# Kernel tuning notes

Measured on AMD Instinct MI355X. Metric: run time of the kernel, lower is better.

Reference implementation:

```python
import jax, jax.numpy as jnp
import numpy as np

NUM_GRAPHS = 512


def setup_inputs() -> dict:
    key = jax.random.key(0)
    ks = jax.random.split(key, 12)
    N, E, D, H, C = 100000, 1600000, 128, 128, 10
    x = jax.random.normal(ks[0], (N, D), dtype=jnp.float32)
    edge_index = jax.random.randint(ks[1], (2, E), 0, N, dtype=jnp.int64)
    batch = jnp.sort(jax.random.randint(ks[2], (N,), 0, NUM_GRAPHS, dtype=jnp.int64))
    def glorot(k, fan_in, fan_out):
        s = jnp.sqrt(6.0 / (fan_in + fan_out))
        return jax.random.uniform(k, (fan_in, fan_out), jnp.float32, -s, s)
    return {
        "x": x, "edge_index": edge_index, "batch": batch,
        "W_init": glorot(ks[3], D, H), "b_init": jnp.zeros((H,), jnp.float32),
        "W_h0": glorot(ks[4], H, H), "b_h0": jnp.zeros((H,), jnp.float32),
        "W_h1": glorot(ks[5], H, H), "b_h1": jnp.zeros((H,), jnp.float32),
        "W_out": glorot(ks[6], H, C), "b_out": jnp.zeros((C,), jnp.float32),
    }


def reference(x, edge_index, batch, W_init, b_init, W_h0, b_h0, W_h1, b_h1, W_out, b_out):
    N = x.shape[0]
    loop = jnp.arange(N, dtype=edge_index.dtype)
    # add self-loops (PyG GCNConv default)
    row = jnp.concatenate([edge_index[0], loop])  # source
    col = jnp.concatenate([edge_index[1], loop])  # target
    # symmetric normalization D^-1/2 (A+I) D^-1/2, degrees on target index
    deg = jax.ops.segment_sum(jnp.ones_like(col, dtype=x.dtype), col, num_segments=N)
    dis = jnp.where(deg > 0, jax.lax.rsqrt(jnp.maximum(deg, 1e-12)), 0.0)
    norm = dis[row] * dis[col]  # [E+N]

    def gcn_conv(h, W, b):
        h = h @ W                                    # linear first (as in PyG)
        msg = h[row] * norm[:, None]                 # gather + scale
        return jax.ops.segment_sum(msg, col, num_segments=N) + b  # scatter-add

    h = jax.nn.relu(gcn_conv(x, W_init, b_init))
    h = jax.nn.relu(gcn_conv(h, W_h0, b_h0))
    h = jax.nn.relu(gcn_conv(h, W_h1, b_h1))
    h = gcn_conv(h, W_out, b_out)
    # global mean pooling over graphs
    sums = jax.ops.segment_sum(h, batch, num_segments=NUM_GRAPHS)
    cnt = jax.ops.segment_sum(jnp.ones((N, 1), h.dtype), batch, num_segments=NUM_GRAPHS)
    return sums / jnp.maximum(cnt, 1.0)
```

## Files before the change

### kernel.cpp

```cpp
#include <hip/hip_runtime.h>


#define SCAN_BLOCKS 64
#define SCAN_THREADS (SCAN_BLOCKS * 256)

typedef unsigned short u16;
typedef unsigned int   u32;
typedef __attribute__((ext_vector_type(8))) short bf16x8;
typedef __attribute__((ext_vector_type(4))) float f32x4;

static __device__ __forceinline__ u16 f2bf(float x) {
    u32 u = __float_as_uint(x);
    u32 r = (u + 0x7fffu + ((u >> 16) & 1u)) >> 16;
    return (u16)r;
}
static __device__ __forceinline__ float bf_lo(u32 p) { return __uint_as_float(p << 16); }
static __device__ __forceinline__ float bf_hi(u32 p) { return __uint_as_float(p & 0xffff0000u); }

__global__ __launch_bounds__(256) void k_count(const int* __restrict__ col, int E,
                                               int* __restrict__ cnt,
                                               u16* __restrict__ rank) {
    int e = blockIdx.x * 256 + threadIdx.x;
    if (e < E) rank[e] = (u16)atomicAdd(&cnt[col[e]], 1);
}

__global__ __launch_bounds__(256) void k_scan1(const int* __restrict__ cnt,
                                               int* __restrict__ tsum, int N) {
    int t = blockIdx.x * 256 + threadIdx.x;
    int strip = (N + SCAN_THREADS - 1) / SCAN_THREADS;
    int s0 = t * strip;
    int s1 = s0 + strip; if (s1 > N) s1 = N;
    int s = 0;
    for (int i = s0; i < s1; ++i) s += (cnt[i] + 3) & ~3;
    tsum[t] = s;
}

__global__ __launch_bounds__(1024) void k_scan2(int* __restrict__ tsum) {
    __shared__ int part[1024];
    int t = threadIdx.x;
    int base = t * 16;
    int local[16];
    int s = 0;
    #pragma unroll
    for (int i = 0; i < 16; ++i) { local[i] = tsum[base + i]; s += local[i]; }
    part[t] = s;
    __syncthreads();
    for (int off = 1; off < 1024; off <<= 1) {
        int v = part[t];
        int add = (t >= off) ? part[t - off] : 0;
        __syncthreads();
        part[t] = v + add;
        __syncthreads();
    }
    int run = (t == 0) ? 0 : part[t - 1];
    #pragma unroll
    for (int i = 0; i < 16; ++i) { int c = local[i]; tsum[base + i] = run; run += c; }
}

__global__ __launch_bounds__(256) void k_scan3(const int* __restrict__ cnt,
                                               const int* __restrict__ tsum,
                                               int* __restrict__ rowptr,
                                               float* __restrict__ dis,
                                               int* __restrict__ csr, int N) {
    int t = blockIdx.x * 256 + threadIdx.x;
    int strip = (N + SCAN_THREADS - 1) / SCAN_THREADS;
    int s0 = t * strip;
    int s1 = s0 + strip; if (s1 > N) s1 = N;
    int run = tsum[t];
    for (int i = s0; i < s1; ++i) {
        int c = cnt[i];
        int r = (c + 3) & ~3;
        rowptr[i] = run;
        for (int p = run + c; p < run + r; ++p) csr[p] = N;
        run += r;
        dis[i] = rsqrtf((float)(c + 1));
    }
    if (t == SCAN_THREADS - 1) rowptr[N] = run;
}

__global__ __launch_bounds__(256) void k_fill(const int* __restrict__ row,
                                              const int* __restrict__ col, int E,
                                              const int* __restrict__ rowptr,
                                              const u16* __restrict__ rank,
                                              int* __restrict__ csr) {
    int e = blockIdx.x * 256 + threadIdx.x;
    if (e < E) {
        int c = col[e];
        csr[rowptr[c] + (int)rank[e]] = row[e];
    }
}

__global__ __launch_bounds__(256) void k_cast(const float* __restrict__ src,
                                              const float* __restrict__ dis,
                                              u16* __restrict__ bX,
                                              u16* __restrict__ bA,
                                              u16* __restrict__ bB, int N) {
    int i = blockIdx.x * 256 + threadIdx.x;
    int total = (N + 1) * 32;
    if (i >= total) return;
    int v = i >> 5;
    if (v < N) {
        float dv = dis[v];
        float4 val = ((const float4*)src)[i];
        ushort4 o;
        o.x = f2bf(dv * val.x); o.y = f2bf(dv * val.y);
        o.z = f2bf(dv * val.z); o.w = f2bf(dv * val.w);
        ((ushort4*)bX)[i] = o;
    } else {
        ushort4 z = {0, 0, 0, 0};
        ((ushort4*)bX)[i] = z;
        ((ushort4*)bA)[i] = z;
        ((ushort4*)bB)[i] = z;
    }
}

__global__ __launch_bounds__(256) void k_wprep4(const float* __restrict__ W0,
                                                const float* __restrict__ W1,
                                                const float* __restrict__ W2,
                                                const float* __restrict__ Wo,
                                                u32* __restrict__ whi,
                                                u32* __restrict__ wlo, int C) {
    if (blockIdx.x < 24) {
        int which = blockIdx.x >> 3;
        const float* W = (which == 0) ? W0 : (which == 1) ? W1 : W2;
        int t = (blockIdx.x & 7) * 256 + threadIdx.x;
        int lane = t & 63;
        int nk = t >> 6;
        int k0 = nk & 3;
        int ntile = nk >> 2;
        int n = ntile * 16 + (lane & 15);
        int kbase = k0 * 32 + (lane >> 4) * 8;
        u32 hi[4], lo[4];
        #pragma unroll
        for (int tt = 0; tt < 4; ++tt) {
            float w0 = W[(kbase + 2 * tt) * 128 + n];
            float w1 = W[(kbase + 2 * tt + 1) * 128 + n];
            u16 h0 = f2bf(w0), h1 = f2bf(w1);
            u16 l0 = f2bf(w0 - __uint_as_float((u32)h0 << 16));
            u16 l1 = f2bf(w1 - __uint_as_float((u32)h1 << 16));
            hi[tt] = (u32)h0 | ((u32)h1 << 16);
            lo[tt] = (u32)l0 | ((u32)l1 << 16);
        }
        uint4 qh = {hi[0], hi[1], hi[2], hi[3]};
        uint4 ql = {lo[0], lo[1], lo[2], lo[3]};
        int base = which * 2048;
        ((uint4*)whi)[base + t] = qh;
        ((uint4*)wlo)[base + t] = ql;
    } else {
        int t = threadIdx.x;
        int lane = t & 63;
        int k0 = t >> 6;
        int n = lane & 15;
        int kbase = k0 * 32 + (lane >> 4) * 8;
        bool vc = (n < C);
        u32 hi[4], lo[4];
        #pragma unroll
        for (int tt = 0; tt < 4; ++tt) {
            float w0 = vc ? Wo[(kbase + 2 * tt) * C + n] : 0.f;
            float w1 = vc ? Wo[(kbase + 2 * tt + 1) * C + n] : 0.f;
            u16 h0 = f2bf(w0), h1 = f2bf(w1);
            u16 l0 = f2bf(w0 - __uint_as_float((u32)h0 << 16));
            u16 l1 = f2bf(w1 - __uint_as_float((u32)h1 << 16));
            hi[tt] = (u32)h0 | ((u32)h1 << 16);
            lo[tt] = (u32)l0 | ((u32)l1 << 16);
        }
        uint4 qh = {hi[0], hi[1], hi[2], hi[3]};
        uint4 ql = {lo[0], lo[1], lo[2], lo[3]};
        ((uint4*)whi)[6144 + t] = qh;
        ((uint4*)wlo)[6144 + t] = ql;
    }
}

__global__ __launch_bounds__(256) void k_fused(const u16* __restrict__ hin,
                                               const u32* __restrict__ whi,
                                               const u32* __restrict__ wlo,
                                               const float* __restrict__ bias,
                                               u16* __restrict__ hout,
                                               const int* __restrict__ rowptr,
                                               const int* __restrict__ csr,
                                               const float* __restrict__ dis,
                                               int N, int scale_out,
                                               int proj,
                                               const u32* __restrict__ pwhi,
                                               const u32* __restrict__ pwlo,
                                               float* __restrict__ tmpC) {
    __shared__ u32 sS[32 * 68];
    __shared__ float dS[32];
    int tid = threadIdx.x;
    int wave = tid >> 6;
    int lane = tid & 63;
    int row0 = blockIdx.x * 32;
    const uint4* hin4 = (const uint4*)hin;

    int grp = lane >> 4;
    int sub = lane & 15;
    #pragma unroll
    for (int jj = 0; jj < 2; ++jj) {
        int rloc = wave * 8 + jj * 4 + grp;
        int row = row0 + rloc;
        bool hR = row < N;
        int ia = 0, rem = 0;
        float dv = 1.f;
        if (hR) {
            ia  = rowptr[row];
            rem = rowptr[row + 1] - ia;
            dv  = dis[row];
        }
        int nself = hR ? row : N;
        uint4 ps = hin4[((u32)nself << 4) + sub];
        float a0 = bf_lo(ps.x), a1 = bf_hi(ps.x);
        float a2 = bf_lo(ps.y), a3 = bf_hi(ps.y);
        float a4 = bf_lo(ps.z), a5 = bf_hi(ps.z);
        float a6 = bf_lo(ps.w), a7 = bf_hi(ps.w);
        int m = rem;
        m = max(m, __shfl_xor(m, 16));
        m = max(m, __shfl_xor(m, 32));
        const int4* cq = (const int4*)(csr + ia);
        for (int k = 0; k < m; k += 8) {
            int4 q0 = cq[(k >> 2)];
            int4 q1 = cq[(k >> 2) + 1];
            bool v0 = k < rem;
            bool v1 = (k + 4) < rem;
            int n0 = v0 ? q0.x : N;
            int n1 = v0 ? q0.y : N;
            int n2 = v0 ? q0.z : N;
            int n3 = v0 ? q0.w : N;
            int n4 = v1 ? q1.x : N;
            int n5 = v1 ? q1.y : N;
            int n6 = v1 ? q1.z : N;
            int n7 = v1 ? q1.w : N;
            uint4 p0 = hin4[((u32)n0 << 4) + sub];
            uint4 p1 = hin4[((u32)n1 << 4) + sub];
            uint4 p2 = hin4[((u32)n2 << 4) + sub];
            uint4 p3 = hin4[((u32)n3 << 4) + sub];
            uint4 p4 = hin4[((u32)n4 << 4) + sub];
            uint4 p5 = hin4[((u32)n5 << 4) + sub];
            uint4 p6 = hin4[((u32)n6 << 4) + sub];
            uint4 p7 = hin4[((u32)n7 << 4) + sub];
            a0 += bf_lo(p0.x) + bf_lo(p1.x) + bf_lo(p2.x) + bf_lo(p3.x);
            a1 += bf_hi(p0.x) + bf_hi(p1.x) + bf_hi(p2.x) + bf_hi(p3.x);
            a2 += bf_lo(p0.y) + bf_lo(p1.y) + bf_lo(p2.y) + bf_lo(p3.y);
            a3 += bf_hi(p0.y) + bf_hi(p1.y) + bf_hi(p2.y) + bf_hi(p3.y);
            a4 += bf_lo(p0.z) + bf_lo(p1.z) + bf_lo(p2.z) + bf_lo(p3.z);
            a5 += bf_hi(p0.z) + bf_hi(p1.z) + bf_hi(p2.z) + bf_hi(p3.z);
            a6 += bf_lo(p0.w) + bf_lo(p1.w) + bf_lo(p2.w) + bf_lo(p3.w);
            a7 += bf_hi(p0.w) + bf_hi(p1.w) + bf_hi(p2.w) + bf_hi(p3.w);
            a0 += bf_lo(p4.x) + bf_lo(p5.x) + bf_lo(p6.x) + bf_lo(p7.x);
            a1 += bf_hi(p4.x) + bf_hi(p5.x) + bf_hi(p6.x) + bf_hi(p7.x);
            a2 += bf_lo(p4.y) + bf_lo(p5.y) + bf_lo(p6.y) + bf_lo(p7.y);
            a3 += bf_hi(p4.y) + bf_hi(p5.y) + bf_hi(p6.y) + bf_hi(p7.y);
            a4 += bf_lo(p4.z) + bf_lo(p5.z) + bf_lo(p6.z) + bf_lo(p7.z);
            a5 += bf_hi(p4.z) + bf_hi(p5.z) + bf_hi(p6.z) + bf_hi(p7.z);
            a6 += bf_lo(p4.w) + bf_lo(p5.w) + bf_lo(p6.w) + bf_lo(p7.w);
            a7 += bf_hi(p4.w) + bf_hi(p5.w) + bf_hi(p6.w) + bf_hi(p7.w);
        }
        u32 w0 = (u32)f2bf(dv * a0) | ((u32)f2bf(dv * a1) << 16);
        u32 w1 = (u32)f2bf(dv * a2) | ((u32)f2bf(dv * a3) << 16);
        u32 w2 = (u32)f2bf(dv * a4) | ((u32)f2bf(dv * a5) << 16);
        u32 w3 = (u32)f2bf(dv * a6) | ((u32)f2bf(dv * a7) << 16);
        sS[rloc * 65 + sub * 4 + 0] = w0;
        sS[rloc * 65 + sub * 4 + 1] = w1;
        sS[rloc * 65 + sub * 4 + 2] = w2;
        sS[rloc * 65 + sub * 4 + 3] = w3;
        if (sub == 0) dS[rloc] = dv;
    }
    __syncthreads();

    f32x4 acc[2][2] = {{{0.f,0.f,0.f,0.f},{0.f,0.f,0.f,0.f}},
                       {{0.f,0.f,0.f,0.f},{0.f,0.f,0.f,0.f}}};
    int mA = lane & 15;
    int qA = lane >> 4;
    #pragma unroll
    for (int k0 = 0; k0 < 4; ++k0) {
        union { u32 u[4]; bf16x8 v; } A0, A1;
        int ub = k0 * 16 + qA * 4;
        #pragma unroll
        for (int tt = 0; tt < 4; ++tt) {
            A0.u[tt] = sS[mA * 65 + ub + tt];
            A1.u[tt] = sS[(mA + 16) * 65 + ub + tt];
        }
        #pragma unroll
        for (int ct = 0; ct < 2; ++ct) {
            int ntk = ((2 * wave + ct) * 4 + k0) * 64 + lane;
            union { uint4 q; bf16x8 v; } BH, BL;
            BH.q = ((const uint4*)whi)[ntk];
            BL.q = ((const uint4*)wlo)[ntk];
            acc[0][ct] = __builtin_amdgcn_mfma_f32_16x16x32_bf16(A0.v, BH.v, acc[0][ct], 0, 0, 0);
            acc[0][ct] = __builtin_amdgcn_mfma_f32_16x16x32_bf16(A0.v, BL.v, acc[0][ct], 0, 0, 0);
            acc[1][ct] = __builtin_amdgcn_mfma_f32_16x16x32_bf16(A1.v, BH.v, acc[1][ct], 0, 0, 0);
            acc[1][ct] = __builtin_amdgcn_mfma_f32_16x16x32_bf16(A1.v, BL.v, acc[1][ct], 0, 0, 0);
        }
    }

    if (!proj) {
        #pragma unroll
        for (int rt = 0; rt < 2; ++rt) {
            #pragma unroll
            for (int ct = 0; ct < 2; ++ct) {
                int col = (2 * wave + ct) * 16 + (lane & 15);
                float bb = bias[col];
                #pragma unroll
                for (int r = 0; r < 4; ++r) {
                    int rloc = rt * 16 + (lane >> 4) * 4 + r;
                    int row = row0 + rloc;
                    if (row < N) {
                        float o = fmaxf(acc[rt][ct][r] + bb, 0.f);
                        if (scale_out) o *= dS[rloc];
                        hout[((u32)row << 7) + col] = f2bf(o);
                    }
                }
            }
        }
    } else {
        __syncthreads();
        u16* hS16 = (u16*)sS;
        #pragma unroll
        for (int rt = 0; rt < 2; ++rt) {
            #pragma unroll
            for (int ct = 0; ct < 2; ++ct) {
                int col = (2 * wave + ct) * 16 + (lane & 15);
                float bb = bias[col];
                #pragma unroll
                for (int r = 0; r < 4; ++r) {
                    int rloc = rt * 16 + (lane >> 4) * 4 + r;
                    hS16[rloc * 136 + col] = f2bf(fmaxf(acc[rt][ct][r] + bb, 0.f));
                }
            }
        }
        __syncthreads();
        if (wave < 2) {
            int m2 = lane & 15;
            int quad = lane >> 4;
            f32x4 a2 = {0.f, 0.f, 0.f, 0.f};
            #pragma unroll
            for (int k0 = 0; k0 < 4; ++k0) {
                bf16x8 Afrag = *(bf16x8*)&hS16[(wave * 16 + m2) * 136 + k0 * 32 + quad * 8];
                union { uint4 q; bf16x8 v; } BH, BL;
                BH.q = ((const uint4*)pwhi)[k0 * 64 + lane];
                BL.q = ((const uint4*)pwlo)[k0 * 64 + lane];
                a2 = __builtin_amdgcn_mfma_f32_16x16x32_bf16(Afrag, BH.v, a2, 0, 0, 0);
                a2 = __builtin_amdgcn_mfma_f32_16x16x32_bf16(Afrag, BL.v, a2, 0, 0, 0);
            }
            #pragma unroll
            for (int r = 0; r < 4; ++r) {
                int rloc = wave * 16 + quad * 4 + r;
                int row = row0 + rloc;
                if (row < N) tmpC[((u32)row << 4) + m2] = a2[r] * dS[rloc];
            }
        }
        if (blockIdx.x == 0 && tid < 16) tmpC[((u32)N << 4) + tid] = 0.f;
    }
}

__global__ __launch_bounds__(256) void k_aggpool(const float* __restrict__ tp,
                                                 const int* __restrict__ rowptr,
                                                 const int* __restrict__ csr,
                                                 const float* __restrict__ dis,
                                                 const int* __restrict__ batch,
                                                 const float* __restrict__ bout,
                                                 float* __restrict__ out,
                                                 int N, int C) {
    __shared__ float red[256];
    int g = blockIdx.x;
    int tid = threadIdx.x;
    int c = tid & 15;
    int rg = tid >> 4;
    int lo = 0, hi = N;
    while (lo < hi) { int m = (lo + hi) >> 1; if (batch[m] < g) lo = m + 1; else hi = m; }
    int lb = lo;
    hi = N;
    while (lo < hi) { int m = (lo + hi) >> 1; if (batch[m] <= g) lo = m + 1; else hi = m; }
    int ub = lo;
    const int4* csr4 = (const int4*)csr;
    float pacc = 0.f;
    for (int v = lb + rg; v < ub; v += 16) {
        float acc = tp[((u32)v << 4) + c];
        int i = rowptr[v], e = rowptr[v + 1];
        for (; i + 8 <= e; i += 8) {
            int4 q0 = csr4[(u32)i >> 2];
            int4 q1 = csr4[((u32)i >> 2) + 1];
            acc += tp[((u32)q0.x << 4) + c] + tp[((u32)q0.y << 4) + c]
                 + tp[((u32)q0.z << 4) + c] + tp[((u32)q0.w << 4) + c]
                 + tp[((u32)q1.x << 4) + c] + tp[((u32)q1.y << 4) + c]
                 + tp[((u32)q1.z << 4) + c] + tp[((u32)q1.w << 4) + c];
        }
        if (i < e) {
            int4 q0 = csr4[(u32)i >> 2];
            acc += tp[((u32)q0.x << 4) + c] + tp[((u32)q0.y << 4) + c]
                 + tp[((u32)q0.z << 4) + c] + tp[((u32)q0.w << 4) + c];
        }
        pacc += dis[v] * acc;
    }
    red[tid] = pacc;
    __syncthreads();
    #pragma unroll
    for (int s = 8; s >= 1; s >>= 1) {
        if (rg < s) red[tid] += red[tid + s * 16];
        __syncthreads();
    }
    if (tid < C) {
        float cnt = (float)(ub - lb);
        out[g * C + tid] = (red[tid] + cnt * bout[tid]) / fmaxf(cnt, 1.0f);
    }
}

extern "C" void kernel_launch(void* const* d_in, const int* in_sizes, int n_in,
                              void* d_out, int out_size, void* d_ws, size_t ws_size,
                              hipStream_t stream) {
    const float* x      = (const float*)d_in[0];
    const int*   ei     = (const int*)d_in[1];
    const int*   batch  = (const int*)d_in[2];
    const float* W_init = (const float*)d_in[3];
    const float* b_init = (const float*)d_in[4];
    const float* W_h0   = (const float*)d_in[5];
    const float* b_h0   = (const float*)d_in[6];
    const float* W_h1   = (const float*)d_in[7];
    const float* b_h1   = (const float*)d_in[8];
    const float* W_out  = (const float*)d_in[9];
    const float* b_out  = (const float*)d_in[10];

    int N = in_sizes[0] / 128;
    int E = in_sizes[1] / 2;
    int C = in_sizes[10];
    int G = out_size / C;

    size_t off = 0;
    auto alloc = [&](size_t bytes) -> char* {
        char* p = (char*)d_ws + off;
        off += (bytes + 255) & ~(size_t)255;
        return p;
    };
    u16*   bufX   = (u16*)  alloc((size_t)(N + 1) * 128 * 2);
    u16*   bufA   = (u16*)  alloc((size_t)(N + 1) * 128 * 2);
    u16*   bufB   = (u16*)  alloc((size_t)(N + 1) * 128 * 2);
    float* dis    = (float*)alloc((size_t)N * 4);
    int*   rowptr = (int*)  alloc((size_t)(N + 1) * 4);
    int*   csr    = (int*)  alloc(((size_t)E + 3 * (size_t)N + 8) * 4);
    int*   tsum   = (int*)  alloc((size_t)SCAN_THREADS * 4);
    u32*   whi    = (u32*)  alloc((3 * 2048 + 256) * 16);
    u32*   wlo    = (u32*)  alloc((3 * 2048 + 256) * 16);
    size_t zoff   = off;
    int*   cnt    = (int*)  alloc((size_t)N * 4);
    size_t zbytes = off - zoff;

    u16*   rank   = (u16*)bufB;
    float* tmpC   = (float*)bufX;

    hipMemsetAsync(cnt, 0, zbytes, stream);

    const int* rowi = ei;
    const int* coli = ei + E;

    int eb = (E + 255) / 256;
    k_count<<<eb, 256, 0, stream>>>(coli, E, cnt, rank);
    k_scan1<<<SCAN_BLOCKS, 256, 0, stream>>>(cnt, tsum, N);
    k_scan2<<<1, 1024, 0, stream>>>(tsum);
    k_scan3<<<SCAN_BLOCKS, 256, 0, stream>>>(cnt, tsum, rowptr, dis, csr, N);
    k_fill<<<eb, 256, 0, stream>>>(rowi, coli, E, rowptr, rank, csr);

    k_wprep4<<<25, 256, 0, stream>>>(W_init, W_h0, W_h1, W_out, whi, wlo, C);

    int cg = ((N + 1) * 32 + 255) / 256;
    k_cast<<<cg, 256, 0, stream>>>(x, dis, bufX, bufA, bufB, N);

    int fb = (N + 31) / 32;

    k_fused<<<fb, 256, 0, stream>>>(bufX, whi,         wlo,         b_init, bufA, rowptr, csr, dis, N, 1, 0, nullptr, nullptr, nullptr);
    k_fused<<<fb, 256, 0, stream>>>(bufA, whi + 8192,  wlo + 8192,  b_h0,   bufB, rowptr, csr, dis, N, 1, 0, nullptr, nullptr, nullptr);
    k_fused<<<fb, 256, 0, stream>>>(bufB, whi + 16384, wlo + 16384, b_h1,   bufA, rowptr, csr, dis, N, 0, 1, whi + 24576, wlo + 24576, tmpC);

    k_aggpool<<<G, 256, 0, stream>>>(tmpC, rowptr, csr, dis, batch, b_out, (float*)d_out, N, C);
}
```

Before: 468.0 us.

## Bucket CSR neighbors by source-node shard and widen pooling blocks

CSR construction now counts edges per (destination, source shard) pair, with shards of 4096 source IDs, and places each edge at a per-shard segment base. Neighbor lists therefore come out roughly sorted by source index, which should give better cache locality for the gathers in the aggregation kernels. The cost is a count array of N*SH entries (about 25 per node) that must be memset, scanned and read, which adds a lot of memory traffic to the preprocessing. The pooling kernel also grows from 256 to 1024 threads per graph block.

Measured after the change: 544.4 us. 1.16x slower.

```diff
diff --git a/kernel.cpp b/kernel.cpp
--- a/kernel.cpp
+++ b/kernel.cpp
@@ -3,6 +3,7 @@
 
 #define SCAN_BLOCKS 64
 #define SCAN_THREADS (SCAN_BLOCKS * 256)
+#define SHARD_SHIFT 12
 
 typedef unsigned short u16;
 typedef unsigned int   u32;
@@ -17,21 +18,31 @@
 static __device__ __forceinline__ float bf_lo(u32 p) { return __uint_as_float(p << 16); }
 static __device__ __forceinline__ float bf_hi(u32 p) { return __uint_as_float(p & 0xffff0000u); }
 
-__global__ __launch_bounds__(256) void k_count(const int* __restrict__ col, int E,
-                                               int* __restrict__ cnt,
+__global__ __launch_bounds__(256) void k_count(const int* __restrict__ col,
+                                               const int* __restrict__ row,
+                                               int E,
+                                               int* __restrict__ cnt32, int SH,
                                                u16* __restrict__ rank) {
     int e = blockIdx.x * 256 + threadIdx.x;
-    if (e < E) rank[e] = (u16)atomicAdd(&cnt[col[e]], 1);
-}
-
-__global__ __launch_bounds__(256) void k_scan1(const int* __restrict__ cnt,
+    if (e < E) {
+        int c = col[e];
+        int s = row[e] >> SHARD_SHIFT;
+        rank[e] = (u16)atomicAdd(&cnt32[c * SH + s], 1);
+    }
+}
+
+__global__ __launch_bounds__(256) void k_scan1(const int* __restrict__ cnt32, int SH,
                                                int* __restrict__ tsum, int N) {
     int t = blockIdx.x * 256 + threadIdx.x;
     int strip = (N + SCAN_THREADS - 1) / SCAN_THREADS;
     int s0 = t * strip;
     int s1 = s0 + strip; if (s1 > N) s1 = N;
     int s = 0;
-    for (int i = s0; i < s1; ++i) s += (cnt[i] + 3) & ~3;
+    for (int i = s0; i < s1; ++i) {
+        int tot = 0;
+        for (int q = 0; q < SH; ++q) tot += cnt32[i * SH + q];
+        s += (tot + 3) & ~3;
+    }
     tsum[t] = s;
 }
 
@@ -57,9 +68,10 @@
     for (int i = 0; i < 16; ++i) { int c = local[i]; tsum[base + i] = run; run += c; }
 }
 
-__global__ __launch_bounds__(256) void k_scan3(const int* __restrict__ cnt,
+__global__ __launch_bounds__(256) void k_scan3(const int* __restrict__ cnt32, int SH,
                                                const int* __restrict__ tsum,
                                                int* __restrict__ rowptr,
+                                               int* __restrict__ segbase,
                                                float* __restrict__ dis,
                                                int* __restrict__ csr, int N) {
     int t = blockIdx.x * 256 + threadIdx.x;
@@ -68,9 +80,14 @@
     int s1 = s0 + strip; if (s1 > N) s1 = N;
     int run = tsum[t];
     for (int i = s0; i < s1; ++i) {
-        int c = cnt[i];
+        rowptr[i] = run;
+        int acc = 0;
+        for (int q = 0; q < SH; ++q) {
+            segbase[i * SH + q] = run + acc;
+            acc += cnt32[i * SH + q];
+        }
+        int c = acc;
         int r = (c + 3) & ~3;
-        rowptr[i] = run;
         for (int p = run + c; p < run + r; ++p) csr[p] = N;
         run += r;
         dis[i] = rsqrtf((float)(c + 1));
@@ -80,13 +97,15 @@
 
 __global__ __launch_bounds__(256) void k_fill(const int* __restrict__ row,
                                               const int* __restrict__ col, int E,
-                                              const int* __restrict__ rowptr,
+                                              const int* __restrict__ segbase, int SH,
                                               const u16* __restrict__ rank,
                                               int* __restrict__ csr) {
     int e = blockIdx.x * 256 + threadIdx.x;
     if (e < E) {
         int c = col[e];
-        csr[rowptr[c] + (int)rank[e]] = row[e];
+        int src = row[e];
+        int s = src >> SHARD_SHIFT;
+        csr[segbase[c * SH + s] + (int)rank[e]] = src;
     }
 }
 
@@ -352,15 +371,15 @@
     }
 }
 
-__global__ __launch_bounds__(256) void k_aggpool(const float* __restrict__ tp,
-                                                 const int* __restrict__ rowptr,
-                                                 const int* __restrict__ csr,
-                                                 const float* __restrict__ dis,
-                                                 const int* __restrict__ batch,
-                                                 const float* __restrict__ bout,
-                                                 float* __restrict__ out,
-                                                 int N, int C) {
-    __shared__ float red[256];
+__global__ __launch_bounds__(1024) void k_aggpool(const float* __restrict__ tp,
+                                                  const int* __restrict__ rowptr,
+                                                  const int* __restrict__ csr,
+                                                  const float* __restrict__ dis,
+                                                  const int* __restrict__ batch,
+                                                  const float* __restrict__ bout,
+                                                  float* __restrict__ out,
+                                                  int N, int C) {
+    __shared__ float red[1024];
     int g = blockIdx.x;
     int tid = threadIdx.x;
     int c = tid & 15;
@@ -373,7 +392,7 @@
     int ub = lo;
     const int4* csr4 = (const int4*)csr;
     float pacc = 0.f;
-    for (int v = lb + rg; v < ub; v += 16) {
+    for (int v = lb + rg; v < ub; v += 64) {
         float acc = tp[((u32)v << 4) + c];
         int i = rowptr[v], e = rowptr[v + 1];
         for (; i + 8 <= e; i += 8) {
@@ -394,7 +413,7 @@
     red[tid] = pacc;
     __syncthreads();
     #pragma unroll
-    for (int s = 8; s >= 1; s >>= 1) {
+    for (int s = 32; s >= 1; s >>= 1) {
         if (rg < s) red[tid] += red[tid + s * 16];
         __syncthreads();
     }
@@ -423,6 +442,7 @@
     int E = in_sizes[1] / 2;
     int C = in_sizes[10];
     int G = out_size / C;
+    int SH = (N >> SHARD_SHIFT) + 1;
 
     size_t off = 0;
     auto alloc = [&](size_t bytes) -> char* {
@@ -439,24 +459,25 @@
     int*   tsum   = (int*)  alloc((size_t)SCAN_THREADS * 4);
     u32*   whi    = (u32*)  alloc((3 * 2048 + 256) * 16);
     u32*   wlo    = (u32*)  alloc((3 * 2048 + 256) * 16);
+    int*   segbase= (int*)  alloc((size_t)N * SH * 4);
     size_t zoff   = off;
-    int*   cnt    = (int*)  alloc((size_t)N * 4);
+    int*   cnt32  = (int*)  alloc((size_t)N * SH * 4);
     size_t zbytes = off - zoff;
 
     u16*   rank   = (u16*)bufB;
     float* tmpC   = (float*)bufX;
 
-    hipMemsetAsync(cnt, 0, zbytes, stream);
+    hipMemsetAsync(cnt32, 0, zbytes, stream);
 
     const int* rowi = ei;
     const int* coli = ei + E;
 
     int eb = (E + 255) / 256;
-    k_count<<<eb, 256, 0, stream>>>(coli, E, cnt, rank);
-    k_scan1<<<SCAN_BLOCKS, 256, 0, stream>>>(cnt, tsum, N);
+    k_count<<<eb, 256, 0, stream>>>(coli, rowi, E, cnt32, SH, rank);
+    k_scan1<<<SCAN_BLOCKS, 256, 0, stream>>>(cnt32, SH, tsum, N);
     k_scan2<<<1, 1024, 0, stream>>>(tsum);
-    k_scan3<<<SCAN_BLOCKS, 256, 0, stream>>>(cnt, tsum, rowptr, dis, csr, N);
-    k_fill<<<eb, 256, 0, stream>>>(rowi, coli, E, rowptr, rank, csr);
+    k_scan3<<<SCAN_BLOCKS, 256, 0, stream>>>(cnt32, SH, tsum, rowptr, segbase, dis, csr, N);
+    k_fill<<<eb, 256, 0, stream>>>(rowi, coli, E, segbase, SH, rank, csr);
 
     k_wprep4<<<25, 256, 0, stream>>>(W_init, W_h0, W_h1, W_out, whi, wlo, C);
 
@@ -469,5 +490,5 @@
     k_fused<<<fb, 256, 0, stream>>>(bufA, whi + 8192,  wlo + 8192,  b_h0,   bufB, rowptr, csr, dis, N, 1, 0, nullptr, nullptr, nullptr);
     k_fused<<<fb, 256, 0, stream>>>(bufB, whi + 16384, wlo + 16384, b_h1,   bufA, rowptr, csr, dis, N, 0, 1, whi + 24576, wlo + 24576, tmpC);
 
-    k_aggpool<<<G, 256, 0, stream>>>(tmpC, rowptr, csr, dis, batch, b_out, (float*)d_out, N, C);
-}
+    k_aggpool<<<G, 1024, 0, stream>>>(tmpC, rowptr, csr, dis, batch, b_out, (float*)d_out, N, C);
+}
```

## Store final projection in bf16 and widen aggregate-pool blocks to 1024 threads

Applied to the files above, without the earlier changes.

The final-layer projected features (16 channels per node) are now written as bf16 instead of fp32, halving the bytes gathered per edge in the pooling aggregation. The aggpool kernel reads two channels per 32-bit load, uses 8 lanes per node and 128 nodes in flight per graph, and runs 1024-thread blocks with a deeper shared-memory reduction. This should cut gather traffic and raise memory-level parallelism per graph, at the cost of bf16 rounding on the last-layer messages before aggregation.

New measurement: 438.3 us. -6.3%, faster.

```diff
diff --git a/kernel.cpp b/kernel.cpp
--- a/kernel.cpp
+++ b/kernel.cpp
@@ -183,7 +183,7 @@
                                                int proj,
                                                const u32* __restrict__ pwhi,
                                                const u32* __restrict__ pwlo,
-                                               float* __restrict__ tmpC) {
+                                               u16* __restrict__ tmpC) {
     __shared__ u32 sS[32 * 68];
     __shared__ float dS[32];
     int tid = threadIdx.x;
@@ -345,26 +345,27 @@
             for (int r = 0; r < 4; ++r) {
                 int rloc = wave * 16 + quad * 4 + r;
                 int row = row0 + rloc;
-                if (row < N) tmpC[((u32)row << 4) + m2] = a2[r] * dS[rloc];
+                if (row < N) tmpC[((u32)row << 4) + m2] = f2bf(a2[r] * dS[rloc]);
             }
         }
-        if (blockIdx.x == 0 && tid < 16) tmpC[((u32)N << 4) + tid] = 0.f;
-    }
-}
-
-__global__ __launch_bounds__(256) void k_aggpool(const float* __restrict__ tp,
-                                                 const int* __restrict__ rowptr,
-                                                 const int* __restrict__ csr,
-                                                 const float* __restrict__ dis,
-                                                 const int* __restrict__ batch,
-                                                 const float* __restrict__ bout,
-                                                 float* __restrict__ out,
-                                                 int N, int C) {
-    __shared__ float red[256];
+        if (blockIdx.x == 0 && tid < 16) tmpC[((u32)N << 4) + tid] = 0;
+    }
+}
+
+__global__ __launch_bounds__(1024) void k_aggpool(const u16* __restrict__ tp,
+                                                  const int* __restrict__ rowptr,
+                                                  const int* __restrict__ csr,
+                                                  const float* __restrict__ dis,
+                                                  const int* __restrict__ batch,
+                                                  const float* __restrict__ bout,
+                                                  float* __restrict__ out,
+                                                  int N, int C) {
+    __shared__ float2 red[1024];
     int g = blockIdx.x;
     int tid = threadIdx.x;
-    int c = tid & 15;
-    int rg = tid >> 4;
+    int c = tid & 7;
+    int rg = tid >> 3;
+    const u32* tp32 = (const u32*)tp;
     int lo = 0, hi = N;
     while (lo < hi) { int m = (lo + hi) >> 1; if (batch[m] < g) lo = m + 1; else hi = m; }
     int lb = lo;
@@ -372,35 +373,57 @@
     while (lo < hi) { int m = (lo + hi) >> 1; if (batch[m] <= g) lo = m + 1; else hi = m; }
     int ub = lo;
     const int4* csr4 = (const int4*)csr;
-    float pacc = 0.f;
-    for (int v = lb + rg; v < ub; v += 16) {
-        float acc = tp[((u32)v << 4) + c];
+    float px = 0.f, py = 0.f;
+    for (int v = lb + rg; v < ub; v += 128) {
+        u32 ps = tp32[((u32)v << 3) + c];
+        float ax = bf_lo(ps), ay = bf_hi(ps);
         int i = rowptr[v], e = rowptr[v + 1];
         for (; i + 8 <= e; i += 8) {
             int4 q0 = csr4[(u32)i >> 2];
             int4 q1 = csr4[((u32)i >> 2) + 1];
-            acc += tp[((u32)q0.x << 4) + c] + tp[((u32)q0.y << 4) + c]
-                 + tp[((u32)q0.z << 4) + c] + tp[((u32)q0.w << 4) + c]
-                 + tp[((u32)q1.x << 4) + c] + tp[((u32)q1.y << 4) + c]
-                 + tp[((u32)q1.z << 4) + c] + tp[((u32)q1.w << 4) + c];
+            u32 p0 = tp32[((u32)q0.x << 3) + c];
+            u32 p1 = tp32[((u32)q0.y << 3) + c];
+            u32 p2 = tp32[((u32)q0.z << 3) + c];
+            u32 p3 = tp32[((u32)q0.w << 3) + c];
+            u32 p4 = tp32[((u32)q1.x << 3) + c];
+            u32 p5 = tp32[((u32)q1.y << 3) + c];
+            u32 p6 = tp32[((u32)q1.z << 3) + c];
+            u32 p7 = tp32[((u32)q1.w << 3) + c];
+            ax += bf_lo(p0) + bf_lo(p1) + bf_lo(p2) + bf_lo(p3)
+                + bf_lo(p4) + bf_lo(p5) + bf_lo(p6) + bf_lo(p7);
+            ay += bf_hi(p0) + bf_hi(p1) + bf_hi(p2) + bf_hi(p3)
+                + bf_hi(p4) + bf_hi(p5) + bf_hi(p6) + bf_hi(p7);
         }
         if (i < e) {
             int4 q0 = csr4[(u32)i >> 2];
-            acc += tp[((u32)q0.x << 4) + c] + tp[((u32)q0.y << 4) + c]
-                 + tp[((u32)q0.z << 4) + c] + tp[((u32)q0.w << 4) + c];
-        }
-        pacc += dis[v] * acc;
-    }
-    red[tid] = pacc;
+            u32 p0 = tp32[((u32)q0.x << 3) + c];
+            u32 p1 = tp32[((u32)q0.y << 3) + c];
+            u32 p2 = tp32[((u32)q0.z << 3) + c];
+            u32 p3 = tp32[((u32)q0.w << 3) + c];
+            ax += bf_lo(p0) + bf_lo(p1) + bf_lo(p2) + bf_lo(p3);
+            ay += bf_hi(p0) + bf_hi(p1) + bf_hi(p2) + bf_hi(p3);
+        }
+        float dv = dis[v];
+        px += dv * ax;
+        py += dv * ay;
+    }
+    red[tid] = make_float2(px, py);
     __syncthreads();
     #pragma unroll
-    for (int s = 8; s >= 1; s >>= 1) {
-        if (rg < s) red[tid] += red[tid + s * 16];
+    for (int s = 64; s >= 1; s >>= 1) {
+        if (rg < s) {
+            float2 o = red[tid + s * 8];
+            red[tid].x += o.x; red[tid].y += o.y;
+        }
         __syncthreads();
     }
-    if (tid < C) {
+    if (tid < 8) {
         float cnt = (float)(ub - lb);
-        out[g * C + tid] = (red[tid] + cnt * bout[tid]) / fmaxf(cnt, 1.0f);
+        float den = fmaxf(cnt, 1.0f);
+        float2 s2 = red[tid];
+        int ch0 = 2 * tid, ch1 = 2 * tid + 1;
+        if (ch0 < C) out[g * C + ch0] = (s2.x + cnt * bout[ch0]) / den;
+        if (ch1 < C) out[g * C + ch1] = (s2.y + cnt * bout[ch1]) / den;
     }
 }
 
@@ -444,7 +467,7 @@
     size_t zbytes = off - zoff;
 
     u16*   rank   = (u16*)bufB;
-    float* tmpC   = (float*)bufX;
+    u16*   tmpC   = (u16*)bufX;
 
     hipMemsetAsync(cnt, 0, zbytes, stream);
 
@@ -469,5 +492,5 @@
     k_fused<<<fb, 256, 0, stream>>>(bufA, whi + 8192,  wlo + 8192,  b_h0,   bufB, rowptr, csr, dis, N, 1, 0, nullptr, nullptr, nullptr);
     k_fused<<<fb, 256, 0, stream>>>(bufB, whi + 16384, wlo + 16384, b_h1,   bufA, rowptr, csr, dis, N, 0, 1, whi + 24576, wlo + 24576, tmpC);
 
-    k_aggpool<<<G, 256, 0, stream>>>(tmpC, rowptr, csr, dis, batch, b_out, (float*)d_out, N, C);
-}
+    k_aggpool<<<G, 1024, 0, stream>>>(tmpC, rowptr, csr, dis, batch, b_out, (float*)d_out, N, C);
+}
```
